# Kernel optimization log

Measured on AMD Instinct MI355X. Metric: run time of the kernel, lower is better.

The kernel has to match this reference:

```python
import jax, jax.numpy as jnp
import numpy as np

B, L, D = 4, 2048, 1024
H, HD = 16, 64
N = 2048  # total number of sets across the batch
TOPK = 8


def setup_inputs() -> dict:
    key = jax.random.key(0)
    ks = jax.random.split(key, 10)
    s = 0.02
    # ragged segment pointers: roughly equal segments with jitter, min length >= TOPK
    rng = np.random.default_rng(0)
    base = N // B
    jit = rng.integers(-base // 4, base // 4, size=B)
    lens = np.maximum(base + jit, TOPK + 1)
    lens = (lens * (N / lens.sum())).astype(np.int64)
    lens[-1] = N - lens[:-1].sum()
    q_ptrs = jnp.asarray(np.concatenate([[0], np.cumsum(lens)]), dtype=jnp.int64)
    return {
        "token_states": jax.random.normal(ks[0], (B, L, D), jnp.float32),
        "Z_sets": jax.random.normal(ks[1], (N, H, HD), jnp.float32),
        "desc_q": jax.random.normal(ks[2], (N, D), jnp.float32),
        "q_ptrs": q_ptrs,
        "Wg_w": jax.random.normal(ks[3], (D, D), jnp.float32) * s,
        "Wg_b": jnp.zeros((D,), jnp.float32),
        "Wd_w": jax.random.normal(ks[4], (D, D), jnp.float32) * s,
        "Wd_b": jnp.zeros((D,), jnp.float32),
        "out_w": jax.random.normal(ks[5], (D, D), jnp.float32) * s,
        "out_b": jnp.zeros((D,), jnp.float32),
    }


def reference(token_states, Z_sets, desc_q, q_ptrs, Wg_w, Wg_b, Wd_w, Wd_b, out_w, out_b):
    Bs, Ls, Ds = token_states.shape
    Ns = desc_q.shape[0]
    S = Ns  # static pad width (upper bound on max segment length)
    starts = q_ptrs[:-1]                       # [B]
    lengths = q_ptrs[1:] - starts              # [B]
    pos = jnp.arange(S)
    idx = jnp.clip(starts[:, None] + pos[None, :], 0, Ns - 1)   # [B,S]
    valid = pos[None, :] < lengths[:, None]                      # [B,S] bool
    desc_pad = jnp.where(valid[..., None], desc_q[idx], 0.0)     # [B,S,D]
    z_pad = jnp.where(valid[..., None, None], Z_sets[idx], 0.0)  # [B,S,H,HD]

    Tproj = token_states @ Wg_w.T + Wg_b                         # [B,L,D]
    Dproj = desc_pad @ Wd_w.T + Wd_b                             # [B,S,D]
    logits = jnp.einsum('bld,bsd->bls', Tproj, Dproj)            # [B,L,S]
    logits = jnp.where(valid[:, None, :], logits, -jnp.inf)

    if TOPK > 0 and S > TOPK:
        vals, tidx = jax.lax.top_k(logits, TOPK)                 # [B,L,K]
        bidx = jnp.arange(Bs)[:, None, None]
        lidx = jnp.arange(Ls)[None, :, None]
        tmp = jnp.full_like(logits, -jnp.inf)
        tmp = tmp.at[bidx, lidx, tidx].set(vals)
        gates = jax.nn.softmax(tmp, axis=-1)
    else:
        gates = jax.nn.softmax(logits, axis=-1)

    mix = jnp.einsum('bls,bshd->blhd', gates, z_pad)             # [B,L,H,HD]
    return mix.reshape(Bs, Ls, Ds) @ out_w.T + out_b
```

## Files before the change

### kernel.cpp

```cpp
#include <hip/hip_runtime.h>
#include <hip/hip_bf16.h>
#include <math.h>

#define BQ    4
#define LQ    2048
#define D_DIM 1024
#define NQ    2048
#define SMAX  1024
#define TOPK  8

typedef __attribute__((ext_vector_type(8))) short          short8;
typedef __attribute__((ext_vector_type(8))) _Float16       half8;
typedef __attribute__((ext_vector_type(4))) float          f32x4;
typedef __attribute__((ext_vector_type(8))) unsigned short ushort8;
typedef __attribute__((ext_vector_type(4))) unsigned short ushort4v;

typedef __attribute__((address_space(3))) void as3_void;
typedef __attribute__((address_space(1))) void as1_void;

__device__ __forceinline__ void gload_lds16(const void* g, void* l) {
    __builtin_amdgcn_global_load_lds((const as1_void*)g, (as3_void*)l, 16, 0, 0);
}

__device__ __forceinline__ unsigned short f2bf(float f) {
    __hip_bfloat16 h = __float2bfloat16(f);
    return *reinterpret_cast<unsigned short*>(&h);
}
__device__ __forceinline__ float bf2f(unsigned short u) {
    unsigned int w = (unsigned int)u << 16;
    return *reinterpret_cast<float*>(&w);
}
__device__ __forceinline__ unsigned short f2h(float f) {
    _Float16 h = (_Float16)f;
    return *reinterpret_cast<unsigned short*>(&h);
}
__device__ __forceinline__ float h2f(unsigned short u) {
    _Float16 h = *reinterpret_cast<_Float16*>(&u);
    return (float)h;
}

__device__ __forceinline__ int swz(int r) { return (r ^ (r >> 2)) & 3; }

#define WAIT_VM0   asm volatile("s_waitcnt vmcnt(0)" ::: "memory")
#define WAIT_VM3   asm volatile("s_waitcnt vmcnt(3)" ::: "memory")
#define WAIT_VM4   asm volatile("s_waitcnt vmcnt(4)" ::: "memory")
#define WAIT_VM6   asm volatile("s_waitcnt vmcnt(6)" ::: "memory")
#define WAIT_LGKM0 asm volatile("s_waitcnt lgkmcnt(0)" ::: "memory")

__global__ __launch_bounds__(256) void k_cvt_all(
    const float* __restrict__ token_states, const float* __restrict__ desc_q,
    const float* __restrict__ Wd_w, const float* __restrict__ out_w,
    const float* __restrict__ Z_sets, const int* __restrict__ q_raw,
    unsigned short* __restrict__ tokenH, unsigned short* __restrict__ tokenL,
    unsigned short* __restrict__ descH,  unsigned short* __restrict__ descL,
    unsigned short* __restrict__ wdh,    unsigned short* __restrict__ owb,
    unsigned short* __restrict__ Zb,     int* __restrict__ qp)
{
    const int blk = blockIdx.x;
    if (blk == 0 && threadIdx.x == 0) {
        bool is64 = (q_raw[1] == 0);
        for (int i = 0; i <= BQ; ++i)
            qp[i] = is64 ? q_raw[2 * i] : q_raw[i];
    }

    const float* in; unsigned short *hi, *lo = nullptr; int local; bool fp16m = true;
    if (blk < 4096)      { in = token_states; hi = tokenH; lo = tokenL; local = blk; }
    else if (blk < 5120) { in = desc_q; hi = descH; lo = descL; local = blk - 4096; }
    else if (blk < 5632) { in = Wd_w;   hi = wdh;   local = blk - 5120; }
    else if (blk < 6144) { in = out_w;  hi = owb;   local = blk - 5632; fp16m = false; }
    else                 { in = Z_sets; hi = Zb;    local = blk - 6144; fp16m = false; }

    int i = (local * 256 + threadIdx.x) * 8;
    float4 v0 = *reinterpret_cast<const float4*>(in + i);
    float4 v1 = *reinterpret_cast<const float4*>(in + i + 4);
    float x[8] = {v0.x, v0.y, v0.z, v0.w, v1.x, v1.y, v1.z, v1.w};
    ushort8 h8, l8;
#pragma unroll
    for (int k = 0; k < 8; ++k) {
        if (fp16m) {
            unsigned short h = f2h(x[k]);
            h8[k] = h;
            l8[k] = f2h(x[k] - h2f(h));
        } else {
            h8[k] = f2bf(x[k]);
        }
    }
    *reinterpret_cast<ushort8*>(hi + i) = h8;
    if (lo) *reinterpret_cast<ushort8*>(lo + i) = l8;
}

__global__ __launch_bounds__(256) void k_wgt(
    const float* __restrict__ Wg, unsigned short* __restrict__ wgT)
{
    __shared__ float t[64][65];
    const int tid = threadIdx.x;
    const int j0 = (blockIdx.x & 15) * 64;
    const int d0 = (blockIdx.x >> 4) * 64;
#pragma unroll
    for (int i = 0; i < 16; ++i) {
        int r = i * 4 + (tid >> 6);
        int c = tid & 63;
        t[r][c] = Wg[(size_t)(d0 + r) * D_DIM + j0 + c];
    }
    __syncthreads();
#pragma unroll
    for (int i = 0; i < 16; ++i) {
        int jj = i * 4 + (tid >> 6);
        int dd = tid & 63;
        wgT[(size_t)(j0 + jj) * D_DIM + d0 + dd] = f2h(t[dd][jj]);
    }
}

__global__ __launch_bounds__(256) void k_dzw(
    const unsigned short* __restrict__ descH, const unsigned short* __restrict__ descL,
    const unsigned short* __restrict__ wdh,
    const float* __restrict__ Wd_b, unsigned short* __restrict__ Dproj16,
    const unsigned short* __restrict__ Zb, const unsigned short* __restrict__ owb,
    unsigned short* __restrict__ ZWb)
{
    constexpr int K = D_DIM, N = D_DIM;
    __shared__ __align__(16) char lds[2 * 24576];

    const int d = blockIdx.x;
    const int sub = d >> 1;
    const int bcol = (sub & 7) * 128;
    const int brow = (sub >> 3) * 128;

    const int tid = threadIdx.x;
    const int ln  = tid & 63;
    const int wid = tid >> 6;
    const int wm  = wid >> 1, wn = wid & 1;
    const int fr  = ln & 15, fs = ln >> 4;
    const int srow = tid >> 2;
    const int sslt = tid & 3;

    const int kk0 = (sslt ^ swz(srow)) << 3;
    const size_t offA0 = (size_t)(brow + srow) * K + kk0;
    const size_t offW0 = (size_t)(bcol + srow) * K + kk0;

    if ((d & 1) == 0) {
        auto stage = [&](char* base, int k0) {
            gload_lds16(descH + offA0 + k0,          base + wid * 1024);
            gload_lds16(descH + offA0 + 64 * K + k0, base + 4096 + wid * 1024);
            gload_lds16(descL + offA0 + k0,          base + 8192 + wid * 1024);
            gload_lds16(descL + offA0 + 64 * K + k0, base + 12288 + wid * 1024);
            gload_lds16(wdh + offW0 + k0,            base + 16384 + wid * 1024);
            gload_lds16(wdh + offW0 + 64 * K + k0,   base + 20480 + wid * 1024);
        };

        f32x4 acc[4][4] = {};
        stage(lds, 0);
        stage(lds + 24576, 32);

        const int NT = K / 32;
        for (int t = 0; t < NT; ++t) {
            if (t < NT - 1) { WAIT_VM6; } else { WAIT_VM0; }
            __builtin_amdgcn_s_barrier();

            char* base = lds + (t & 1) * 24576;
            half8 ahf[4], alf[4], bhf[4];
#pragma unroll
            for (int mi = 0; mi < 4; ++mi) {
                int r = wm * 64 + mi * 16 + fr;
                int o = r * 64 + ((fs ^ swz(r)) << 4);
                ahf[mi] = *reinterpret_cast<const half8*>(base + o);
                alf[mi] = *reinterpret_cast<const half8*>(base + 8192 + o);
            }
#pragma unroll
            for (int ni = 0; ni < 4; ++ni) {
                int c = wn * 64 + ni * 16 + fr;
                int o = c * 64 + ((fs ^ swz(c)) << 4);
                bhf[ni] = *reinterpret_cast<const half8*>(base + 16384 + o);
            }
            __builtin_amdgcn_s_setprio(1);
#pragma unroll
            for (int mi = 0; mi < 4; ++mi)
#pragma unroll
                for (int ni = 0; ni < 4; ++ni)
                    acc[mi][ni] = __builtin_amdgcn_mfma_f32_16x16x32_f16(
                        ahf[mi], bhf[ni], acc[mi][ni], 0, 0, 0);
#pragma unroll
            for (int mi = 0; mi < 4; ++mi)
#pragma unroll
                for (int ni = 0; ni < 4; ++ni)
                    acc[mi][ni] = __builtin_amdgcn_mfma_f32_16x16x32_f16(
                        alf[mi], bhf[ni], acc[mi][ni], 0, 0, 0);
            __builtin_amdgcn_s_setprio(0);

            WAIT_LGKM0;
            __builtin_amdgcn_s_barrier();
            if (t + 2 < NT) stage(base, (t + 2) * 32);
        }

        float bv[4];
#pragma unroll
        for (int ni = 0; ni < 4; ++ni)
            bv[ni] = Wd_b[bcol + wn * 64 + ni * 16 + fr];

#pragma unroll
        for (int mi = 0; mi < 4; ++mi) {
#pragma unroll
            for (int reg = 0; reg < 4; ++reg) {
                int row = brow + wm * 64 + mi * 16 + fs * 4 + reg;
#pragma unroll
                for (int ni = 0; ni < 4; ++ni) {
                    int col = bcol + wn * 64 + ni * 16 + fr;
                    Dproj16[(size_t)row * N + col] = f2h(acc[mi][ni][reg] + bv[ni]);
                }
            }
        }
    } else {
        auto stage = [&](char* base, int k0) {
            gload_lds16(Zb + offA0 + k0,           base + wid * 1024);
            gload_lds16(Zb + offA0 + 64 * K + k0,  base + 4096 + wid * 1024);
            gload_lds16(owb + offW0 + k0,          base + 8192 + wid * 1024);
            gload_lds16(owb + offW0 + 64 * K + k0, base + 12288 + wid * 1024);
        };

        f32x4 acc[4][4] = {};
        stage(lds, 0);
        stage(lds + 24576, 32);

        const int NT = K / 32;
        for (int t = 0; t < NT; ++t) {
            if (t < NT - 1) { WAIT_VM4; } else { WAIT_VM0; }
            __builtin_amdgcn_s_barrier();

            char* base = lds + (t & 1) * 24576;
            short8 a[4], b[4];
#pragma unroll
            for (int mi = 0; mi < 4; ++mi) {
                int r = wm * 64 + mi * 16 + fr;
                a[mi] = *reinterpret_cast<const short8*>(base + r * 64 + ((fs ^ swz(r)) << 4));
            }
#pragma unroll
            for (int ni = 0; ni < 4; ++ni) {
                int c = wn * 64 + ni * 16 + fr;
                b[ni] = *reinterpret_cast<const short8*>(base + 8192 + c * 64 + ((fs ^ swz(c)) << 4));
            }
            __builtin_amdgcn_s_setprio(1);
#pragma unroll
            for (int mi = 0; mi < 4; ++mi)
#pragma unroll
                for (int ni = 0; ni < 4; ++ni)
                    acc[mi][ni] = __builtin_amdgcn_mfma_f32_16x16x32_bf16(
                        a[mi], b[ni], acc[mi][ni], 0, 0, 0);
            __builtin_amdgcn_s_setprio(0);

            WAIT_LGKM0;
            __builtin_amdgcn_s_barrier();
            if (t + 2 < NT) stage(base, (t + 2) * 32);
        }

#pragma unroll
        for (int mi = 0; mi < 4; ++mi) {
#pragma unroll
            for (int reg = 0; reg < 4; ++reg) {
                int row = brow + wm * 64 + mi * 16 + fs * 4 + reg;
#pragma unroll
                for (int ni = 0; ni < 4; ++ni) {
                    int col = bcol + wn * 64 + ni * 16 + fr;
                    ZWb[(size_t)row * N + col] = f2bf(acc[mi][ni][reg]);
                }
            }
        }
    }
}

__global__ __launch_bounds__(256) void k_g(
    const unsigned short* __restrict__ A, const unsigned short* __restrict__ W,
    unsigned short* __restrict__ C, int M, int N, int K)
{
    __shared__ __align__(16) char lds[2 * 16384];

    const int nbx = gridDim.x;
    const int total = nbx * gridDim.y;
    const int d = blockIdx.x + nbx * blockIdx.y;
    const int logical = (d & 7) * (total >> 3) + (d >> 3);
    const int bcol = (logical % nbx) * 128;
    const int brow = (logical / nbx) * 128;

    const int tid = threadIdx.x;
    const int ln  = tid & 63;
    const int wid = tid >> 6;
    const int wm  = wid >> 1, wn = wid & 1;
    const int fr  = ln & 15, fs = ln >> 4;
    const int srow = tid >> 2;
    const int sslt = tid & 3;

    const int kk0 = (sslt ^ swz(srow)) << 3;
    const size_t offA0 = (size_t)(brow + srow) * K + kk0;
    const size_t offW0 = (size_t)(bcol + srow) * K + kk0;

    auto stage = [&](char* base, int k0) {
        gload_lds16(A + offA0 + k0,          base + wid * 1024);
        gload_lds16(A + offA0 + 64 * K + k0, base + 4096 + wid * 1024);
        gload_lds16(W + offW0 + k0,          base + 8192 + wid * 1024);
        gload_lds16(W + offW0 + 64 * K + k0, base + 12288 + wid * 1024);
    };

    f32x4 acc[4][4] = {};

    stage(lds, 0);
    stage(lds + 16384, 32);

    const int NT = K / 32;
    for (int t = 0; t < NT; ++t) {
        if (t < NT - 1) { WAIT_VM4; } else { WAIT_VM0; }
        __builtin_amdgcn_s_barrier();

        char* base = lds + (t & 1) * 16384;
        half8 a[4], b[4];
#pragma unroll
        for (int mi = 0; mi < 4; ++mi) {
            int r = wm * 64 + mi * 16 + fr;
            a[mi] = *reinterpret_cast<const half8*>(base + r * 64 + ((fs ^ swz(r)) << 4));
        }
#pragma unroll
        for (int ni = 0; ni < 4; ++ni) {
            int c = wn * 64 + ni * 16 + fr;
            b[ni] = *reinterpret_cast<const half8*>(base + 8192 + c * 64 + ((fs ^ swz(c)) << 4));
        }
        __builtin_amdgcn_s_setprio(1);
#pragma unroll
        for (int mi = 0; mi < 4; ++mi)
#pragma unroll
            for (int ni = 0; ni < 4; ++ni)
                acc[mi][ni] = __builtin_amdgcn_mfma_f32_16x16x32_f16(
                    a[mi], b[ni], acc[mi][ni], 0, 0, 0);
        __builtin_amdgcn_s_setprio(0);

        WAIT_LGKM0;
        __builtin_amdgcn_s_barrier();
        if (t + 2 < NT) stage(base, (t + 2) * 32);
    }

#pragma unroll
    for (int mi = 0; mi < 4; ++mi) {
#pragma unroll
        for (int reg = 0; reg < 4; ++reg) {
            int row = brow + wm * 64 + mi * 16 + fs * 4 + reg;
#pragma unroll
            for (int ni = 0; ni < 4; ++ni) {
                int col = bcol + wn * 64 + ni * 16 + fr;
                C[(size_t)row * N + col] = f2h(acc[mi][ni][reg]);
            }
        }
    }
}

__global__ __launch_bounds__(256) void k_cvec(
    const unsigned short* __restrict__ Dproj16, const float* __restrict__ bg,
    const int* __restrict__ qp, int* __restrict__ tmap, float* __restrict__ c)
{
    if (blockIdx.x == 0 && threadIdx.x == 0) {
        int idx = 0;
        for (int b = 0; b < BQ; ++b) {
            int len = qp[b + 1] - qp[b];
            int nt = (len + 63) >> 6;
            for (int j = 0; j < nt; ++j)
                tmap[idx++] = (b << 16) | (j * 64);
        }
        tmap[40] = idx;
    }

    const int row = blockIdx.x * 4 + (threadIdx.x >> 6);
    const int ln  = threadIdx.x & 63;
    const unsigned short* dr = Dproj16 + (size_t)row * D_DIM + ln * 16;
    float s = 0.f;
#pragma unroll
    for (int h = 0; h < 2; ++h) {
        ushort8 v = *reinterpret_cast<const ushort8*>(dr + h * 8);
#pragma unroll
        for (int j = 0; j < 8; ++j)
            s = fmaf(bg[ln * 16 + h * 8 + j], h2f(v[j]), s);
    }
#pragma unroll
    for (int off = 32; off > 0; off >>= 1)
        s += __shfl_xor(s, off);
    if (ln == 0) c[row] = s;
}

__global__ __launch_bounds__(256) void k_logits_2p(
    const unsigned short* __restrict__ TH, const unsigned short* __restrict__ TL,
    const unsigned short* __restrict__ G16, const float* __restrict__ cvec,
    const int* __restrict__ qp, const int* __restrict__ tmap,
    float* __restrict__ logits)
{
    const int d = blockIdx.x + 40 * blockIdx.y;
    const int logical = (d & 7) * 160 + (d >> 3);
    const int t0   = logical % 40;
    const int brow = (logical / 40) * 64;
    if (t0 >= tmap[40]) return;
    const int m    = tmap[t0];
    const int b    = m >> 16;
    const int bcol = m & 0xffff;
    const int start = qp[b];

    __shared__ __align__(16) char lds[2 * 12288];

    const int tid = threadIdx.x;
    const int ln  = tid & 63;
    const int wid = tid >> 6;
    const int fr  = ln & 15, fs = ln >> 4;
    const int srow = tid >> 2;
    const int sslt = tid & 3;

    const int kka = (sslt ^ swz(srow)) << 3;
    const size_t offA0 = ((size_t)b * LQ + brow + srow) * D_DIM + kka;
    int wr = start + bcol + srow; if (wr > NQ - 1) wr = NQ - 1;
    const size_t offW0 = (size_t)wr * D_DIM + kka;

    auto stage = [&](char* base, int k0) {
        gload_lds16(TH + offA0 + k0,  base + wid * 1024);
        gload_lds16(TL + offA0 + k0,  base + 4096 + wid * 1024);
        gload_lds16(G16 + offW0 + k0, base + 8192 + wid * 1024);
    };

    f32x4 acc[4] = {};

    stage(lds, 0);
    stage(lds + 12288, 32);

    const int NT = D_DIM / 32;
    for (int t = 0; t < NT; ++t) {
        if (t < NT - 1) { WAIT_VM3; } else { WAIT_VM0; }
        __builtin_amdgcn_s_barrier();

        char* base = lds + (t & 1) * 12288;
        half8 ah, al, bf[4];
        {
            int r = wid * 16 + fr;
            int o = r * 64 + ((fs ^ swz(r)) << 4);
            ah = *reinterpret_cast<const half8*>(base + o);
            al = *reinterpret_cast<const half8*>(base + 4096 + o);
        }
#pragma unroll
        for (int ni = 0; ni < 4; ++ni) {
            int cc = ni * 16 + fr;
            bf[ni] = *reinterpret_cast<const half8*>(base + 8192 + cc * 64 + ((fs ^ swz(cc)) << 4));
        }
        __builtin_amdgcn_s_setprio(1);
#pragma unroll
        for (int ni = 0; ni < 4; ++ni)
            acc[ni] = __builtin_amdgcn_mfma_f32_16x16x32_f16(ah, bf[ni], acc[ni], 0, 0, 0);
#pragma unroll
        for (int ni = 0; ni < 4; ++ni)
            acc[ni] = __builtin_amdgcn_mfma_f32_16x16x32_f16(al, bf[ni], acc[ni], 0, 0, 0);
        __builtin_amdgcn_s_setprio(0);

        WAIT_LGKM0;
        __builtin_amdgcn_s_barrier();
        if (t + 2 < NT) stage(base, (t + 2) * 32);
    }

    float cv[4];
#pragma unroll
    for (int ni = 0; ni < 4; ++ni) {
        int ci = start + bcol + ni * 16 + fr;
        if (ci > NQ - 1) ci = NQ - 1;
        cv[ni] = cvec[ci];
    }

#pragma unroll
    for (int reg = 0; reg < 4; ++reg) {
        size_t row = (size_t)b * LQ + brow + wid * 16 + fs * 4 + reg;
#pragma unroll
        for (int ni = 0; ni < 4; ++ni) {
            int col = bcol + ni * 16 + fr;
            logits[row * SMAX + col] = acc[ni][reg] + cv[ni];
        }
    }
}

__global__ __launch_bounds__(256) void k_topk_out(
    const float* __restrict__ logits, const unsigned short* __restrict__ ZW,
    const float* __restrict__ out_b, const int* __restrict__ qp,
    float* __restrict__ out)
{
    const int ln  = threadIdx.x & 63;
    const int row = blockIdx.x * 4 + (threadIdx.x >> 6);
    const int b   = row >> 11;
    const int start = qp[b], len = qp[b + 1] - start;

    const float* lrow = logits + (size_t)row * SMAX;

    float v[16];
#pragma unroll
    for (int c = 0; c < 4; ++c) {
        float4 q = reinterpret_cast<const float4*>(lrow)[c * 64 + ln];
        int s0 = c * 256 + ln * 4;
        v[c * 4 + 0] = (s0 + 0 < len) ? q.x : -INFINITY;
        v[c * 4 + 1] = (s0 + 1 < len) ? q.y : -INFINITY;
        v[c * 4 + 2] = (s0 + 2 < len) ? q.z : -INFINITY;
        v[c * 4 + 3] = (s0 + 3 < len) ? q.w : -INFINITY;
    }

    float wv[TOPK]; int wi[TOPK];
#pragma unroll
    for (int it = 0; it < TOPK; ++it) {
        float bvv = v[0]; int bj = 0;
#pragma unroll
        for (int j = 1; j < 16; ++j)
            if (v[j] > bvv) { bvv = v[j]; bj = j; }
        int gidx = (bj >> 2) * 256 + ln * 4 + (bj & 3);
        float cv = bvv; int ci = gidx;
#pragma unroll
        for (int off = 32; off > 0; off >>= 1) {
            float ov = __shfl_xor(cv, off);
            int   oi = __shfl_xor(ci, off);
            if (ov > cv || (ov == cv && oi < ci)) { cv = ov; ci = oi; }
        }
        wv[it] = cv; wi[it] = ci;
#pragma unroll
        for (int j = 0; j < 16; ++j) {
            int sj = (j >> 2) * 256 + ln * 4 + (j & 3);
            if (sj == ci) v[j] = -INFINITY;
        }
    }

    float m = wv[0], denom = 0.f;
    float g[TOPK];
#pragma unroll
    for (int k = 0; k < TOPK; ++k) { g[k] = expf(wv[k] - m); denom += g[k]; }
    float inv = 1.f / denom;

    float4 acc[4];
#pragma unroll
    for (int c = 0; c < 4; ++c)
        acc[c] = reinterpret_cast<const float4*>(out_b)[c * 64 + ln];

#pragma unroll
    for (int k = 0; k < TOPK; ++k) {
        int si = wi[k] >= 0 ? wi[k] : 0;
        const ushort4v* zr = reinterpret_cast<const ushort4v*>(
            ZW + (size_t)(start + si) * D_DIM);
        float wgt = g[k] * inv;
#pragma unroll
        for (int c = 0; c < 4; ++c) {
            ushort4v z = zr[c * 64 + ln];
            acc[c].x = fmaf(wgt, bf2f(z[0]), acc[c].x);
            acc[c].y = fmaf(wgt, bf2f(z[1]), acc[c].y);
            acc[c].z = fmaf(wgt, bf2f(z[2]), acc[c].z);
            acc[c].w = fmaf(wgt, bf2f(z[3]), acc[c].w);
        }
    }
    float* orow = out + (size_t)row * D_DIM;
#pragma unroll
    for (int c = 0; c < 4; ++c)
        reinterpret_cast<float4*>(orow)[c * 64 + ln] = acc[c];
}

extern "C" void kernel_launch(void* const* d_in, const int* in_sizes, int n_in,
                              void* d_out, int out_size, void* d_ws, size_t ws_size,
                              hipStream_t stream) {
    const float* token_states = (const float*)d_in[0];
    const float* Z_sets       = (const float*)d_in[1];
    const float* desc_q       = (const float*)d_in[2];
    const int*   q_raw        = (const int*)d_in[3];
    const float* Wg_w  = (const float*)d_in[4];
    const float* Wg_b  = (const float*)d_in[5];
    const float* Wd_w  = (const float*)d_in[6];
    const float* Wd_b  = (const float*)d_in[7];
    const float* out_w = (const float*)d_in[8];
    const float* out_b = (const float*)d_in[9];
    float* out = (float*)d_out;

    const size_t NTOK = (size_t)BQ * LQ * D_DIM;
    const size_t NDES = (size_t)NQ * D_DIM;
    const size_t NW   = (size_t)D_DIM * D_DIM;

    char* ws = (char*)d_ws;
    int* qp   = (int*)ws;
    int* tmap = (int*)(ws + 64);
    unsigned short* tokenH  = (unsigned short*)(ws + 256);
    unsigned short* tokenL  = tokenH + NTOK;
    unsigned short* descH   = tokenL + NTOK;
    unsigned short* descL   = descH + NDES;
    unsigned short* wdh     = descL + NDES;
    unsigned short* wgT     = wdh + NW;
    unsigned short* owb     = wgT + NW;
    unsigned short* Zb      = owb + NW;
    unsigned short* Dproj16 = Zb + NDES;
    unsigned short* ZWb     = Dproj16 + NDES;
    unsigned short* G16     = ZWb + NDES;
    float* cvec             = (float*)(G16 + NDES);
    float* logit            = cvec + 2048;

    k_cvt_all<<<7168, 256, 0, stream>>>(
        token_states, desc_q, Wd_w, out_w, Z_sets, q_raw,
        tokenH, tokenL, descH, descL, wdh, owb, Zb, qp);

    k_wgt<<<256, 256, 0, stream>>>(Wg_w, wgT);

    k_dzw<<<256, 256, 0, stream>>>(
        descH, descL, wdh, Wd_b, Dproj16, Zb, owb, ZWb);

    k_g<<<dim3(8, 16), 256, 0, stream>>>(Dproj16, wgT, G16, NQ, D_DIM, D_DIM);

    k_cvec<<<512, 256, 0, stream>>>(Dproj16, Wg_b, qp, tmap, cvec);

    k_logits_2p<<<dim3(40, 32), 256, 0, stream>>>(
        tokenH, tokenL, G16, cvec, qp, tmap, logit);

    k_topk_out<<<(BQ * LQ) / 4, 256, 0, stream>>>(logit, ZWb, out_b, qp, out);
}
```

Measured before the change: 133.6 us.

## Merge small kernels into fewer launches and triple-buffer logits GEMM staging

Folds the Wg transpose into the conversion kernel as extra blocks, and merges the G GEMM and cvec reduction into one launch as separate block ranges. This removes two kernel launches and lets the independent work run concurrently. The logits kernel moves from double to triple buffered LDS staging with deeper vmcnt waits, keeping more loads in flight at the cost of more shared memory per block. The extra LDS and the shared __shared__ tile in the conversion kernel may reduce occupancy.

```diff
diff --git a/kernel.cpp b/kernel.cpp
--- a/kernel.cpp
+++ b/kernel.cpp
@@ -50,17 +50,42 @@
 __global__ __launch_bounds__(256) void k_cvt_all(
     const float* __restrict__ token_states, const float* __restrict__ desc_q,
     const float* __restrict__ Wd_w, const float* __restrict__ out_w,
-    const float* __restrict__ Z_sets, const int* __restrict__ q_raw,
+    const float* __restrict__ Z_sets, const float* __restrict__ Wg_w,
+    const int* __restrict__ q_raw,
     unsigned short* __restrict__ tokenH, unsigned short* __restrict__ tokenL,
     unsigned short* __restrict__ descH,  unsigned short* __restrict__ descL,
     unsigned short* __restrict__ wdh,    unsigned short* __restrict__ owb,
-    unsigned short* __restrict__ Zb,     int* __restrict__ qp)
+    unsigned short* __restrict__ Zb,     unsigned short* __restrict__ wgT,
+    int* __restrict__ qp)
 {
+    __shared__ float t[64][65];
     const int blk = blockIdx.x;
-    if (blk == 0 && threadIdx.x == 0) {
+    const int tid = threadIdx.x;
+
+    if (blk == 0 && tid == 0) {
         bool is64 = (q_raw[1] == 0);
         for (int i = 0; i <= BQ; ++i)
             qp[i] = is64 ? q_raw[2 * i] : q_raw[i];
+    }
+
+    if (blk >= 7168) {
+        const int tb = blk - 7168;
+        const int j0 = (tb & 15) * 64;
+        const int d0 = (tb >> 4) * 64;
+#pragma unroll
+        for (int i = 0; i < 16; ++i) {
+            int r = i * 4 + (tid >> 6);
+            int c = tid & 63;
+            t[r][c] = Wg_w[(size_t)(d0 + r) * D_DIM + j0 + c];
+        }
+        __syncthreads();
+#pragma unroll
+        for (int i = 0; i < 16; ++i) {
+            int jj = i * 4 + (tid >> 6);
+            int dd = tid & 63;
+            wgT[(size_t)(j0 + jj) * D_DIM + d0 + dd] = f2h(t[dd][jj]);
+        }
+        return;
     }
 
     const float* in; unsigned short *hi, *lo = nullptr; int local; bool fp16m = true;
@@ -70,7 +95,7 @@
     else if (blk < 6144) { in = out_w;  hi = owb;   local = blk - 5632; fp16m = false; }
     else                 { in = Z_sets; hi = Zb;    local = blk - 6144; fp16m = false; }
 
-    int i = (local * 256 + threadIdx.x) * 8;
+    int i = (local * 256 + tid) * 8;
     float4 v0 = *reinterpret_cast<const float4*>(in + i);
     float4 v1 = *reinterpret_cast<const float4*>(in + i + 4);
     float x[8] = {v0.x, v0.y, v0.z, v0.w, v1.x, v1.y, v1.z, v1.w};
@@ -87,28 +112,6 @@
     }
     *reinterpret_cast<ushort8*>(hi + i) = h8;
     if (lo) *reinterpret_cast<ushort8*>(lo + i) = l8;
-}
-
-__global__ __launch_bounds__(256) void k_wgt(
-    const float* __restrict__ Wg, unsigned short* __restrict__ wgT)
-{
-    __shared__ float t[64][65];
-    const int tid = threadIdx.x;
-    const int j0 = (blockIdx.x & 15) * 64;
-    const int d0 = (blockIdx.x >> 4) * 64;
-#pragma unroll
-    for (int i = 0; i < 16; ++i) {
-        int r = i * 4 + (tid >> 6);
-        int c = tid & 63;
-        t[r][c] = Wg[(size_t)(d0 + r) * D_DIM + j0 + c];
-    }
-    __syncthreads();
-#pragma unroll
-    for (int i = 0; i < 16; ++i) {
-        int jj = i * 4 + (tid >> 6);
-        int dd = tid & 63;
-        wgT[(size_t)(j0 + jj) * D_DIM + d0 + dd] = f2h(t[dd][jj]);
-    }
 }
 
 __global__ __launch_bounds__(256) void k_dzw(
@@ -267,20 +270,51 @@
     }
 }
 
-__global__ __launch_bounds__(256) void k_g(
-    const unsigned short* __restrict__ A, const unsigned short* __restrict__ W,
-    unsigned short* __restrict__ C, int M, int N, int K)
+__global__ __launch_bounds__(256) void k_gc(
+    const unsigned short* __restrict__ Dproj16, const unsigned short* __restrict__ wgT,
+    unsigned short* __restrict__ G16,
+    const float* __restrict__ bg, const int* __restrict__ qp,
+    int* __restrict__ tmap, float* __restrict__ cvec)
 {
+    constexpr int K = D_DIM, N = D_DIM;
     __shared__ __align__(16) char lds[2 * 16384];
 
-    const int nbx = gridDim.x;
-    const int total = nbx * gridDim.y;
-    const int d = blockIdx.x + nbx * blockIdx.y;
-    const int logical = (d & 7) * (total >> 3) + (d >> 3);
-    const int bcol = (logical % nbx) * 128;
-    const int brow = (logical / nbx) * 128;
-
+    const int blk = blockIdx.x;
     const int tid = threadIdx.x;
+
+    if (blk >= 128) {
+        if (blk == 128 && tid == 0) {
+            int idx = 0;
+            for (int b = 0; b < BQ; ++b) {
+                int len = qp[b + 1] - qp[b];
+                int nt = (len + 63) >> 6;
+                for (int j = 0; j < nt; ++j)
+                    tmap[idx++] = (b << 16) | (j * 64);
+            }
+            tmap[40] = idx;
+        }
+        const int row = (blk - 128) * 4 + (tid >> 6);
+        const int ln  = tid & 63;
+        const unsigned short* dr = Dproj16 + (size_t)row * D_DIM + ln * 16;
+        float s = 0.f;
+#pragma unroll
+        for (int h = 0; h < 2; ++h) {
+            ushort8 v = *reinterpret_cast<const ushort8*>(dr + h * 8);
+#pragma unroll
+            for (int j = 0; j < 8; ++j)
+                s = fmaf(bg[ln * 16 + h * 8 + j], h2f(v[j]), s);
+        }
+#pragma unroll
+        for (int off = 32; off > 0; off >>= 1)
+            s += __shfl_xor(s, off);
+        if (ln == 0) cvec[row] = s;
+        return;
+    }
+
+    const int logical = (blk & 7) * 16 + (blk >> 3);
+    const int bcol = (logical & 7) * 128;
+    const int brow = (logical >> 3) * 128;
+
     const int ln  = tid & 63;
     const int wid = tid >> 6;
     const int wm  = wid >> 1, wn = wid & 1;
@@ -293,10 +327,10 @@
     const size_t offW0 = (size_t)(bcol + srow) * K + kk0;
 
     auto stage = [&](char* base, int k0) {
-        gload_lds16(A + offA0 + k0,          base + wid * 1024);
-        gload_lds16(A + offA0 + 64 * K + k0, base + 4096 + wid * 1024);
-        gload_lds16(W + offW0 + k0,          base + 8192 + wid * 1024);
-        gload_lds16(W + offW0 + 64 * K + k0, base + 12288 + wid * 1024);
+        gload_lds16(Dproj16 + offA0 + k0,          base + wid * 1024);
+        gload_lds16(Dproj16 + offA0 + 64 * K + k0, base + 4096 + wid * 1024);
+        gload_lds16(wgT + offW0 + k0,              base + 8192 + wid * 1024);
+        gload_lds16(wgT + offW0 + 64 * K + k0,     base + 12288 + wid * 1024);
     };
 
     f32x4 acc[4][4] = {};
@@ -343,42 +377,10 @@
 #pragma unroll
             for (int ni = 0; ni < 4; ++ni) {
                 int col = bcol + wn * 64 + ni * 16 + fr;
-                C[(size_t)row * N + col] = f2h(acc[mi][ni][reg]);
-            }
-        }
-    }
-}
-
-__global__ __launch_bounds__(256) void k_cvec(
-    const unsigned short* __restrict__ Dproj16, const float* __restrict__ bg,
-    const int* __restrict__ qp, int* __restrict__ tmap, float* __restrict__ c)
-{
-    if (blockIdx.x == 0 && threadIdx.x == 0) {
-        int idx = 0;
-        for (int b = 0; b < BQ; ++b) {
-            int len = qp[b + 1] - qp[b];
-            int nt = (len + 63) >> 6;
-            for (int j = 0; j < nt; ++j)
-                tmap[idx++] = (b << 16) | (j * 64);
-        }
-        tmap[40] = idx;
-    }
-
-    const int row = blockIdx.x * 4 + (threadIdx.x >> 6);
-    const int ln  = threadIdx.x & 63;
-    const unsigned short* dr = Dproj16 + (size_t)row * D_DIM + ln * 16;
-    float s = 0.f;
-#pragma unroll
-    for (int h = 0; h < 2; ++h) {
-        ushort8 v = *reinterpret_cast<const ushort8*>(dr + h * 8);
-#pragma unroll
-        for (int j = 0; j < 8; ++j)
-            s = fmaf(bg[ln * 16 + h * 8 + j], h2f(v[j]), s);
-    }
-#pragma unroll
-    for (int off = 32; off > 0; off >>= 1)
-        s += __shfl_xor(s, off);
-    if (ln == 0) c[row] = s;
+                G16[(size_t)row * N + col] = f2h(acc[mi][ni][reg]);
+            }
+        }
+    }
 }
 
 __global__ __launch_bounds__(256) void k_logits_2p(
@@ -397,7 +399,7 @@
     const int bcol = m & 0xffff;
     const int start = qp[b];
 
-    __shared__ __align__(16) char lds[2 * 12288];
+    __shared__ __align__(16) char lds[3 * 12288];
 
     const int tid = threadIdx.x;
     const int ln  = tid & 63;
@@ -421,13 +423,16 @@
 
     stage(lds, 0);
     stage(lds + 12288, 32);
+    stage(lds + 24576, 64);
 
     const int NT = D_DIM / 32;
     for (int t = 0; t < NT; ++t) {
-        if (t < NT - 1) { WAIT_VM3; } else { WAIT_VM0; }
+        if (t < NT - 2)      { WAIT_VM6; }
+        else if (t == NT - 2){ WAIT_VM3; }
+        else                 { WAIT_VM0; }
         __builtin_amdgcn_s_barrier();
 
-        char* base = lds + (t & 1) * 12288;
+        char* base = lds + (t % 3) * 12288;
         half8 ah, al, bf[4];
         {
             int r = wid * 16 + fr;
@@ -451,7 +456,7 @@
 
         WAIT_LGKM0;
         __builtin_amdgcn_s_barrier();
-        if (t + 2 < NT) stage(base, (t + 2) * 32);
+        if (t + 3 < NT) stage(base, (t + 3) * 32);
     }
 
     float cv[4];
@@ -587,18 +592,15 @@
     float* cvec             = (float*)(G16 + NDES);
     float* logit            = cvec + 2048;
 
-    k_cvt_all<<<7168, 256, 0, stream>>>(
-        token_states, desc_q, Wd_w, out_w, Z_sets, q_raw,
-        tokenH, tokenL, descH, descL, wdh, owb, Zb, qp);
-
-    k_wgt<<<256, 256, 0, stream>>>(Wg_w, wgT);
+    k_cvt_all<<<7424, 256, 0, stream>>>(
+        token_states, desc_q, Wd_w, out_w, Z_sets, Wg_w, q_raw,
+        tokenH, tokenL, descH, descL, wdh, owb, Zb, wgT, qp);
 
     k_dzw<<<256, 256, 0, stream>>>(
         descH, descL, wdh, Wd_b, Dproj16, Zb, owb, ZWb);
 
-    k_g<<<dim3(8, 16), 256, 0, stream>>>(Dproj16, wgT, G16, NQ, D_DIM, D_DIM);
-
-    k_cvec<<<512, 256, 0, stream>>>(Dproj16, Wg_b, qp, tmap, cvec);
+    k_gc<<<640, 256, 0, stream>>>(
+        Dproj16, wgT, G16, Wg_b, qp, tmap, cvec);
 
     k_logits_2p<<<dim3(40, 32), 256, 0, stream>>>(
         tokenH, tokenL, G16, cvec, qp, tmap, logit);
```

Measured after the change: 131.2 us. No clear change (-1.8%).
